# Kernel optimization log

Measured on AMD Instinct MI355X. Metric: run time of the kernel, lower is better.

The kernel has to match this reference:

```python
import jax, jax.numpy as jnp
import numpy as np

E = 8          # n_routed_experts
D = 2048       # model dim
I = 1408       # moe_inter_dim
K = 2          # n_activated_experts (top-k)
T = 4096       # num tokens


def setup_inputs() -> dict:
    key = jax.random.key(0)
    k1, k2, k3, k4, k5 = jax.random.split(key, 5)
    x = jax.random.normal(k1, (T, D), dtype=jnp.float32)
    token_mask = jnp.ones((T,), dtype=bool)
    weights = jax.random.uniform(k2, (T, K), dtype=jnp.float32)
    indices = jax.random.randint(k3, (T, K), 0, E)
    init_std = 0.02
    gate_and_up_projs = jax.random.normal(k4, (E, D, 2 * I), dtype=jnp.float32) * init_std
    down_projs = jax.random.normal(k5, (E, I, D), dtype=jnp.float32) * init_std
    return {
        "x": x,
        "token_mask": token_mask,
        "weights": weights,
        "indices": indices,
        "gate_and_up_projs": gate_and_up_projs,
        "down_projs": down_projs,
    }


def reference(x, token_mask, weights, indices, gate_and_up_projs, down_projs):
    # Per-expert gate+up projection over all tokens (dense equivalent of the
    # dispatch + grouped-GEMM): [E, T, 2I]
    gu = jnp.einsum("td,edh->eth", x, gate_and_up_projs)
    gate, up = jnp.split(gu, 2, axis=-1)          # swiglu uses torch.chunk(.., 2, -1)
    inter = jax.nn.silu(gate) * up                # [E, T, I]
    y = jnp.einsum("eti,eid->etd", inter, down_projs)  # [E, T, D]
    # Combine: masked tokens (indices filled to -1) contribute nothing -> zero weight
    w_eff = weights * token_mask[:, None].astype(weights.dtype)   # [T, K]
    tok = jnp.arange(T)
    gathered = y[indices, tok[:, None], :]        # [T, K, D]
    out = jnp.einsum("tk,tkd->td", w_eff, gathered)
    return out.astype(x.dtype)
```

## Files before the change

### kernel.cpp

```cpp
#include <hip/hip_runtime.h>
#include <hip/hip_bf16.h>
#include <cstdint>
#include <cstddef>

#define TT 4096
#define DD 2048
#define II 1408
#define EE 8
#define KK 2
#define H2 2816

#define MAXTILES 72
#define BK 32
#define LDK 40

typedef __bf16 bf16x8 __attribute__((ext_vector_type(8)));
typedef float  f32x4  __attribute__((ext_vector_type(4)));

static __device__ __forceinline__ unsigned short f2bf(float f) {
    union { float f; unsigned int u; } v; v.f = f;
    unsigned int u = v.u;
    u += 0x7fffu + ((u >> 16) & 1u);
    return (unsigned short)(u >> 16);
}

static __device__ __forceinline__ bf16x8 ld_frag(const unsigned short* p) {
    return *(const bf16x8*)p;
}

static __device__ __forceinline__ void gload16(const unsigned short* g, unsigned short* l) {
    __builtin_amdgcn_global_load_lds(
        (__attribute__((address_space(1))) void*)(g),
        (__attribute__((address_space(3))) void*)(l),
        16, 0, 0);
}

__global__ __launch_bounds__(256) void k_convert_x(const float* __restrict__ x,
                                                   unsigned short* __restrict__ xb) {
    size_t i = ((size_t)blockIdx.x * 256 + threadIdx.x) * 8;
    const float4* p = (const float4*)(x + i);
    float4 a = p[0], b = p[1];
    uint4 o;
    o.x = (unsigned)f2bf(a.x) | ((unsigned)f2bf(a.y) << 16);
    o.y = (unsigned)f2bf(a.z) | ((unsigned)f2bf(a.w) << 16);
    o.z = (unsigned)f2bf(b.x) | ((unsigned)f2bf(b.y) << 16);
    o.w = (unsigned)f2bf(b.z) | ((unsigned)f2bf(b.w) << 16);
    *(uint4*)(xb + i) = o;
}

__global__ __launch_bounds__(256) void k_tr_cvt(const float* __restrict__ src,
                                                unsigned short* __restrict__ dst,
                                                int K, int H) {
    __shared__ float tile[64][65];
    int e = blockIdx.z;
    int h0 = blockIdx.x * 64, k0 = blockIdx.y * 64;
    const float* s = src + (size_t)e * K * H;
    unsigned short* d = dst + (size_t)e * K * H;
    int t = threadIdx.x;
    #pragma unroll
    for (int i = 0; i < 4; i++) {
        int idx = t + i * 256;
        int r = idx >> 4, c = (idx & 15) * 4;
        float4 v = *(const float4*)(s + (size_t)(k0 + r) * H + h0 + c);
        tile[r][c] = v.x; tile[r][c + 1] = v.y; tile[r][c + 2] = v.z; tile[r][c + 3] = v.w;
    }
    __syncthreads();
    #pragma unroll
    for (int i = 0; i < 4; i++) {
        int idx = t + i * 256;
        int h = idx >> 4, c = (idx & 15) * 4;
        ushort4 o;
        o.x = f2bf(tile[c][h]);     o.y = f2bf(tile[c + 1][h]);
        o.z = f2bf(tile[c + 2][h]); o.w = f2bf(tile[c + 3][h]);
        *(ushort4*)(d + (size_t)(h0 + h) * K + k0 + c) = o;
    }
}

__global__ __launch_bounds__(256) void k_build_lists(const int* __restrict__ indices,
                                                     const float* __restrict__ weights,
                                                     int* __restrict__ cnt,
                                                     int* __restrict__ tok_slab,
                                                     float* __restrict__ w_slab) {
    int g = blockIdx.x * 256 + threadIdx.x;
    if (g >= TT * KK) return;
    int t = g >> 1;
    int e = indices[g];
    float w = weights[g];
    int pos = atomicAdd(&cnt[e], 1);
    tok_slab[e * (TT * KK) + pos] = t;
    w_slab[e * (TT * KK) + pos] = w;
}

__global__ __launch_bounds__(256) void k_build_tiles(const int* __restrict__ cnt,
                                                     const int* __restrict__ tok_slab,
                                                     const float* __restrict__ w_slab,
                                                     int* __restrict__ ctok,
                                                     float* __restrict__ cw,
                                                     int* __restrict__ tr0,
                                                     int* __restrict__ trows,
                                                     int* __restrict__ te) {
    __shared__ int s_off[EE];
    __shared__ int s_cnt[EE];
    if (threadIdx.x == 0) {
        int off = 0, nt = 0;
        for (int e = 0; e < EE; e++) {
            int c = cnt[e];
            s_off[e] = off; s_cnt[e] = c;
            int n = (c + 127) >> 7;
            for (int j = 0; j < n; j++) {
                tr0[nt]   = off + j * 128;
                trows[nt] = min(128, c - j * 128);
                te[nt]    = e;
                nt++;
            }
            off += c;
        }
        for (; nt < MAXTILES; nt++) trows[nt] = 0;
    }
    __syncthreads();
    for (int e = 0; e < EE; e++) {
        int c = s_cnt[e], base = s_off[e];
        for (int i = threadIdx.x; i < c; i += 256) {
            ctok[base + i] = tok_slab[e * (TT * KK) + i];
            cw[base + i]   = w_slab[e * (TT * KK) + i];
        }
    }
}


__global__ __launch_bounds__(256, 2) void k_gemm1_f(const unsigned short* __restrict__ xb,
                                                    const unsigned short* __restrict__ wt1,
                                                    const int* __restrict__ tr0,
                                                    const int* __restrict__ trows,
                                                    const int* __restrict__ te,
                                                    const int* __restrict__ ctok,
                                                    unsigned short* __restrict__ inter) {
    int tile = blockIdx.x;
    int rows = trows[tile];
    if (rows == 0) return;
    int row0 = tr0[tile], e = te[tile], n0 = blockIdx.y * 128;
    int tid = threadIdx.x, wave = tid >> 6, lane = tid & 63;

    __shared__ unsigned short As[128 * 32];
    __shared__ unsigned short Bg[128 * 32];
    __shared__ unsigned short Bu[128 * 32];
    __shared__ int toks[128];

    for (int i = tid; i < 128; i += 256) toks[i] = ctok[row0 + ((i < rows) ? i : 0)];
    __syncthreads();

    int rl = wave * 32 + (lane >> 2);
    int kc = (lane & 3) * 8;
    const unsigned short* gA0 = xb + (size_t)toks[rl] * DD + kc;
    const unsigned short* gA1 = xb + (size_t)toks[rl + 16] * DD + kc;
    const unsigned short* wte = wt1 + (size_t)e * H2 * DD;
    const unsigned short* gBg0 = wte + (size_t)(n0 + rl) * DD + kc;
    const unsigned short* gBg1 = wte + (size_t)(n0 + rl + 16) * DD + kc;
    const unsigned short* gBu0 = gBg0 + (size_t)II * DD;
    const unsigned short* gBu1 = gBg1 + (size_t)II * DD;

    unsigned short* lA0  = &As[(wave * 32) * 32];
    unsigned short* lA1  = &As[(wave * 32 + 16) * 32];
    unsigned short* lBg0 = &Bg[(wave * 32) * 32];
    unsigned short* lBg1 = &Bg[(wave * 32 + 16) * 32];
    unsigned short* lBu0 = &Bu[(wave * 32) * 32];
    unsigned short* lBu1 = &Bu[(wave * 32 + 16) * 32];

    int mb = (wave & 1) * 64, nb = (wave >> 1) * 64;
    int lrow = lane & 15, quad = lane >> 4;

    f32x4 accg[4][4], accu[4][4];
    #pragma unroll
    for (int i = 0; i < 4; i++)
        #pragma unroll
        for (int j = 0; j < 4; j++) { accg[i][j] = (f32x4){0,0,0,0}; accu[i][j] = (f32x4){0,0,0,0}; }

    #pragma unroll 1
    for (int k0 = 0; k0 < DD; k0 += BK) {
        __syncthreads();
        gload16(gA0, lA0);   gload16(gA1, lA1);
        gload16(gBg0, lBg0); gload16(gBg1, lBg1);
        gload16(gBu0, lBu0); gload16(gBu1, lBu1);
        gA0 += BK; gA1 += BK; gBg0 += BK; gBg1 += BK; gBu0 += BK; gBu1 += BK;
        __syncthreads();

        bf16x8 af[4], bg[4], bu[4];
        #pragma unroll
        for (int i = 0; i < 4; i++)
            af[i] = ld_frag(&As[(mb + i * 16 + lrow) * 32 + quad * 8]);
        #pragma unroll
        for (int j = 0; j < 4; j++) {
            bg[j] = ld_frag(&Bg[(nb + j * 16 + lrow) * 32 + quad * 8]);
            bu[j] = ld_frag(&Bu[(nb + j * 16 + lrow) * 32 + quad * 8]);
        }
        #pragma unroll
        for (int i = 0; i < 4; i++)
            #pragma unroll
            for (int j = 0; j < 4; j++) {
                accg[i][j] = __builtin_amdgcn_mfma_f32_16x16x32_bf16(af[i], bg[j], accg[i][j], 0, 0, 0);
                accu[i][j] = __builtin_amdgcn_mfma_f32_16x16x32_bf16(af[i], bu[j], accu[i][j], 0, 0, 0);
            }
    }

    #pragma unroll
    for (int i = 0; i < 4; i++) {
        int rl0 = mb + i * 16 + quad * 4;
        #pragma unroll
        for (int r = 0; r < 4; r++) {
            int rr = rl0 + r;
            if (rr < rows) {
                size_t base = (size_t)(row0 + rr) * II + n0 + nb;
                #pragma unroll
                for (int j = 0; j < 4; j++) {
                    float g = accg[i][j][r], u = accu[i][j][r];
                    float s = g / (1.0f + __expf(-g));
                    inter[base + j * 16 + lrow] = f2bf(s * u);
                }
            }
        }
    }
}

__global__ __launch_bounds__(256, 2) void k_gemm2_f(const unsigned short* __restrict__ inter,
                                                    const unsigned short* __restrict__ wt2,
                                                    const int* __restrict__ tr0,
                                                    const int* __restrict__ trows,
                                                    const int* __restrict__ te,
                                                    const int* __restrict__ ctok,
                                                    const float* __restrict__ cw,
                                                    float* __restrict__ out) {
    int tile = blockIdx.x;
    int rows = trows[tile];
    if (rows == 0) return;
    int row0 = tr0[tile], e = te[tile], n0 = blockIdx.y * 128;
    int tid = threadIdx.x, wave = tid >> 6, lane = tid & 63;

    __shared__ unsigned short As[128 * 32];
    __shared__ unsigned short Bs[128 * 32];
    __shared__ int   toks[128];
    __shared__ float wts[128];

    for (int i = tid; i < 128; i += 256) {
        bool v = (i < rows);
        toks[i] = v ? ctok[row0 + i] : -1;
        wts[i]  = v ? cw[row0 + i] : 0.0f;
    }
    __syncthreads();

    int rl = wave * 32 + (lane >> 2);
    int kc = (lane & 3) * 8;
    int r0c = (rl < rows) ? rl : 0;
    int r1c = (rl + 16 < rows) ? rl + 16 : 0;
    const unsigned short* gA0 = inter + (size_t)(row0 + r0c) * II + kc;
    const unsigned short* gA1 = inter + (size_t)(row0 + r1c) * II + kc;
    const unsigned short* wte = wt2 + (size_t)e * DD * II;
    const unsigned short* gB0 = wte + (size_t)(n0 + rl) * II + kc;
    const unsigned short* gB1 = wte + (size_t)(n0 + rl + 16) * II + kc;

    unsigned short* lA0 = &As[(wave * 32) * 32];
    unsigned short* lA1 = &As[(wave * 32 + 16) * 32];
    unsigned short* lB0 = &Bs[(wave * 32) * 32];
    unsigned short* lB1 = &Bs[(wave * 32 + 16) * 32];

    int mb = (wave & 1) * 64, nb = (wave >> 1) * 64;
    int lrow = lane & 15, quad = lane >> 4;

    f32x4 acc[4][4];
    #pragma unroll
    for (int i = 0; i < 4; i++)
        #pragma unroll
        for (int j = 0; j < 4; j++) acc[i][j] = (f32x4){0,0,0,0};

    #pragma unroll 1
    for (int k0 = 0; k0 < II; k0 += BK) {
        __syncthreads();
        gload16(gA0, lA0); gload16(gA1, lA1);
        gload16(gB0, lB0); gload16(gB1, lB1);
        gA0 += BK; gA1 += BK; gB0 += BK; gB1 += BK;
        __syncthreads();

        bf16x8 af[4], bfg[4];
        #pragma unroll
        for (int i = 0; i < 4; i++)
            af[i] = ld_frag(&As[(mb + i * 16 + lrow) * 32 + quad * 8]);
        #pragma unroll
        for (int j = 0; j < 4; j++)
            bfg[j] = ld_frag(&Bs[(nb + j * 16 + lrow) * 32 + quad * 8]);
        #pragma unroll
        for (int i = 0; i < 4; i++)
            #pragma unroll
            for (int j = 0; j < 4; j++)
                acc[i][j] = __builtin_amdgcn_mfma_f32_16x16x32_bf16(af[i], bfg[j], acc[i][j], 0, 0, 0);
    }

    #pragma unroll
    for (int i = 0; i < 4; i++) {
        int rl0 = mb + i * 16 + quad * 4;
        #pragma unroll
        for (int r = 0; r < 4; r++) {
            int rr = rl0 + r;
            if (rr < rows) {
                int t = toks[rr];
                float w = wts[rr];
                float* op = out + (size_t)t * DD + n0 + nb;
                #pragma unroll
                for (int j = 0; j < 4; j++)
                    unsafeAtomicAdd(op + j * 16 + lrow, w * acc[i][j][r]);
            }
        }
    }
}


__global__ __launch_bounds__(256, 2) void k_gemm1_s(const unsigned short* __restrict__ xb,
                                                    const float* __restrict__ gup,
                                                    const int* __restrict__ tr0,
                                                    const int* __restrict__ trows,
                                                    const int* __restrict__ te,
                                                    const int* __restrict__ ctok,
                                                    unsigned short* __restrict__ inter) {
    int tile = blockIdx.x;
    int rows = trows[tile];
    if (rows == 0) return;
    int row0 = tr0[tile];
    int e    = te[tile];
    int n0   = blockIdx.y * 128;
    int tid  = threadIdx.x;

    __shared__ unsigned short As[128 * LDK];
    __shared__ unsigned short Bg[128 * LDK];
    __shared__ unsigned short Bu[128 * LDK];
    __shared__ int toks[128];

    for (int i = tid; i < 128; i += 256) toks[i] = (i < rows) ? ctok[row0 + i] : -1;

    const float* Wbase = gup + (size_t)e * DD * H2;

    int wave = tid >> 6, lane = tid & 63;
    int mb = (wave & 1) * 64, nb = (wave >> 1) * 64;
    int lrow = lane & 15, quad = lane >> 4;

    f32x4 accg[4][4], accu[4][4];
    #pragma unroll
    for (int i = 0; i < 4; i++)
        #pragma unroll
        for (int j = 0; j < 4; j++) { accg[i][j] = (f32x4){0,0,0,0}; accu[i][j] = (f32x4){0,0,0,0}; }

    #pragma unroll 1
    for (int k0 = 0; k0 < DD; k0 += BK) {
        __syncthreads();
        #pragma unroll
        for (int c = tid; c < 512; c += 256) {
            int r = c >> 2, kk = (c & 3) << 3;
            uint4 v = make_uint4(0, 0, 0, 0);
            int t = toks[r];
            if (t >= 0) v = *(const uint4*)(xb + (size_t)t * DD + k0 + kk);
            *(uint4*)&As[r * LDK + kk] = v;
        }
        #pragma unroll
        for (int c = tid; c < 512; c += 256) {
            int n = c & 127, kcc = (c >> 7) << 3;
            const float* p = Wbase + (size_t)(k0 + kcc) * H2 + (n0 + n);
            unsigned short hg[8], hu[8];
            #pragma unroll
            for (int j = 0; j < 8; j++) {
                hg[j] = f2bf(p[(size_t)j * H2]);
                hu[j] = f2bf(p[(size_t)j * H2 + II]);
            }
            uint4 vg, vu;
            vg.x = (unsigned)hg[0] | ((unsigned)hg[1] << 16);
            vg.y = (unsigned)hg[2] | ((unsigned)hg[3] << 16);
            vg.z = (unsigned)hg[4] | ((unsigned)hg[5] << 16);
            vg.w = (unsigned)hg[6] | ((unsigned)hg[7] << 16);
            vu.x = (unsigned)hu[0] | ((unsigned)hu[1] << 16);
            vu.y = (unsigned)hu[2] | ((unsigned)hu[3] << 16);
            vu.z = (unsigned)hu[4] | ((unsigned)hu[5] << 16);
            vu.w = (unsigned)hu[6] | ((unsigned)hu[7] << 16);
            *(uint4*)&Bg[n * LDK + kcc] = vg;
            *(uint4*)&Bu[n * LDK + kcc] = vu;
        }
        __syncthreads();

        bf16x8 af[4], bg[4], bu[4];
        #pragma unroll
        for (int i = 0; i < 4; i++)
            af[i] = ld_frag(&As[(mb + i * 16 + lrow) * LDK + quad * 8]);
        #pragma unroll
        for (int j = 0; j < 4; j++) {
            bg[j] = ld_frag(&Bg[(nb + j * 16 + lrow) * LDK + quad * 8]);
            bu[j] = ld_frag(&Bu[(nb + j * 16 + lrow) * LDK + quad * 8]);
        }
        #pragma unroll
        for (int i = 0; i < 4; i++)
            #pragma unroll
            for (int j = 0; j < 4; j++) {
                accg[i][j] = __builtin_amdgcn_mfma_f32_16x16x32_bf16(af[i], bg[j], accg[i][j], 0, 0, 0);
                accu[i][j] = __builtin_amdgcn_mfma_f32_16x16x32_bf16(af[i], bu[j], accu[i][j], 0, 0, 0);
            }
    }

    #pragma unroll
    for (int i = 0; i < 4; i++) {
        int rl0 = mb + i * 16 + quad * 4;
        #pragma unroll
        for (int r = 0; r < 4; r++) {
            int rl = rl0 + r;
            if (rl < rows) {
                size_t base = (size_t)(row0 + rl) * II + n0 + nb;
                #pragma unroll
                for (int j = 0; j < 4; j++) {
                    float g = accg[i][j][r], u = accu[i][j][r];
                    float s = g / (1.0f + __expf(-g));
                    inter[base + j * 16 + lrow] = f2bf(s * u);
                }
            }
        }
    }
}

__global__ __launch_bounds__(256, 2) void k_gemm2_s(const unsigned short* __restrict__ inter,
                                                    const float* __restrict__ down,
                                                    const int* __restrict__ tr0,
                                                    const int* __restrict__ trows,
                                                    const int* __restrict__ te,
                                                    const int* __restrict__ ctok,
                                                    const float* __restrict__ cw,
                                                    float* __restrict__ out) {
    int tile = blockIdx.x;
    int rows = trows[tile];
    if (rows == 0) return;
    int row0 = tr0[tile];
    int e    = te[tile];
    int n0   = blockIdx.y * 128;
    int tid  = threadIdx.x;

    __shared__ unsigned short As[128 * LDK];
    __shared__ unsigned short Bs[128 * LDK];
    __shared__ int   toks[128];
    __shared__ float wts[128];

    for (int i = tid; i < 128; i += 256) {
        bool v = (i < rows);
        toks[i] = v ? ctok[row0 + i] : -1;
        wts[i]  = v ? cw[row0 + i] : 0.0f;
    }

    const float* Wbase = down + (size_t)e * II * DD;

    int wave = tid >> 6, lane = tid & 63;
    int mb = (wave & 1) * 64, nb = (wave >> 1) * 64;
    int lrow = lane & 15, quad = lane >> 4;

    f32x4 acc[4][4];
    #pragma unroll
    for (int i = 0; i < 4; i++)
        #pragma unroll
        for (int j = 0; j < 4; j++) acc[i][j] = (f32x4){0,0,0,0};

    #pragma unroll 1
    for (int k0 = 0; k0 < II; k0 += BK) {
        __syncthreads();
        #pragma unroll
        for (int c = tid; c < 512; c += 256) {
            int r = c >> 2, kk = (c & 3) << 3;
            uint4 v = make_uint4(0, 0, 0, 0);
            if (r < rows) v = *(const uint4*)(inter + (size_t)(row0 + r) * II + k0 + kk);
            *(uint4*)&As[r * LDK + kk] = v;
        }
        #pragma unroll
        for (int c = tid; c < 512; c += 256) {
            int n = c & 127, kcc = (c >> 7) << 3;
            const float* p = Wbase + (size_t)(k0 + kcc) * DD + (n0 + n);
            unsigned short h[8];
            #pragma unroll
            for (int j = 0; j < 8; j++) h[j] = f2bf(p[(size_t)j * DD]);
            uint4 v;
            v.x = (unsigned)h[0] | ((unsigned)h[1] << 16);
            v.y = (unsigned)h[2] | ((unsigned)h[3] << 16);
            v.z = (unsigned)h[4] | ((unsigned)h[5] << 16);
            v.w = (unsigned)h[6] | ((unsigned)h[7] << 16);
            *(uint4*)&Bs[n * LDK + kcc] = v;
        }
        __syncthreads();

        bf16x8 af[4], bfg[4];
        #pragma unroll
        for (int i = 0; i < 4; i++)
            af[i] = ld_frag(&As[(mb + i * 16 + lrow) * LDK + quad * 8]);
        #pragma unroll
        for (int j = 0; j < 4; j++)
            bfg[j] = ld_frag(&Bs[(nb + j * 16 + lrow) * LDK + quad * 8]);
        #pragma unroll
        for (int i = 0; i < 4; i++)
            #pragma unroll
            for (int j = 0; j < 4; j++)
                acc[i][j] = __builtin_amdgcn_mfma_f32_16x16x32_bf16(af[i], bfg[j], acc[i][j], 0, 0, 0);
    }

    #pragma unroll
    for (int i = 0; i < 4; i++) {
        int rl0 = mb + i * 16 + quad * 4;
        #pragma unroll
        for (int r = 0; r < 4; r++) {
            int rl = rl0 + r;
            if (rl < rows) {
                int t = toks[rl];
                float w = wts[rl];
                float* op = out + (size_t)t * DD + n0 + nb;
                #pragma unroll
                for (int j = 0; j < 4; j++)
                    unsafeAtomicAdd(op + j * 16 + lrow, w * acc[i][j][r]);
            }
        }
    }
}

constexpr size_t OFF_CNT   = 0;
constexpr size_t OFF_STOK  = 256;
constexpr size_t OFF_SW    = OFF_STOK + (size_t)EE * TT * KK * 4;
constexpr size_t OFF_CTOK  = OFF_SW + (size_t)EE * TT * KK * 4;
constexpr size_t OFF_CW    = OFF_CTOK + (size_t)TT * KK * 4;
constexpr size_t OFF_TR0   = OFF_CW + (size_t)TT * KK * 4;
constexpr size_t OFF_TRS   = OFF_TR0 + 512;
constexpr size_t OFF_TE    = OFF_TRS + 512;
constexpr size_t OFF_XB    = (OFF_TE + 512 + 255) & ~(size_t)255;
constexpr size_t OFF_INTER = OFF_XB + (size_t)TT * DD * 2;
constexpr size_t OFF_WT1   = OFF_INTER + (size_t)TT * KK * II * 2;
constexpr size_t OFF_WT2   = OFF_WT1 + (size_t)EE * H2 * DD * 2;
constexpr size_t WS_SLOW   = OFF_WT1;
constexpr size_t WS_FAST   = OFF_WT2 + (size_t)EE * DD * II * 2;

extern "C" void kernel_launch(void* const* d_in, const int* in_sizes, int n_in,
                              void* d_out, int out_size, void* d_ws, size_t ws_size,
                              hipStream_t stream) {
    const float* x       = (const float*)d_in[0];
    const float* weights = (const float*)d_in[2];
    const int*   indices = (const int*)d_in[3];
    const float* gup     = (const float*)d_in[4];
    const float* down    = (const float*)d_in[5];
    float* out = (float*)d_out;

    if (ws_size < WS_SLOW) return;

    char* ws = (char*)d_ws;
    int*            cnt      = (int*)(ws + OFF_CNT);
    int*            tok_slab = (int*)(ws + OFF_STOK);
    float*          w_slab   = (float*)(ws + OFF_SW);
    int*            ctok     = (int*)(ws + OFF_CTOK);
    float*          cw       = (float*)(ws + OFF_CW);
    int*            tr0      = (int*)(ws + OFF_TR0);
    int*            trows    = (int*)(ws + OFF_TRS);
    int*            te       = (int*)(ws + OFF_TE);
    unsigned short* xb       = (unsigned short*)(ws + OFF_XB);
    unsigned short* inter    = (unsigned short*)(ws + OFF_INTER);
    unsigned short* wt1      = (unsigned short*)(ws + OFF_WT1);
    unsigned short* wt2      = (unsigned short*)(ws + OFF_WT2);

    hipMemsetAsync(cnt, 0, EE * sizeof(int), stream);
    hipMemsetAsync(d_out, 0, (size_t)TT * DD * sizeof(float), stream);

    k_convert_x  <<<dim3((TT * DD) / (256 * 8)), 256, 0, stream>>>(x, xb);
    k_build_lists<<<dim3((TT * KK) / 256), 256, 0, stream>>>(indices, weights, cnt, tok_slab, w_slab);
    k_build_tiles<<<dim3(1), 256, 0, stream>>>(cnt, tok_slab, w_slab, ctok, cw, tr0, trows, te);

    if (ws_size >= WS_FAST) {
        k_tr_cvt<<<dim3(H2 / 64, DD / 64, EE), 256, 0, stream>>>(gup,  wt1, DD, H2);
        k_tr_cvt<<<dim3(DD / 64, II / 64, EE), 256, 0, stream>>>(down, wt2, II, DD);
        k_gemm1_f<<<dim3(MAXTILES, II / 128), 256, 0, stream>>>(xb, wt1, tr0, trows, te, ctok, inter);
        k_gemm2_f<<<dim3(MAXTILES, DD / 128), 256, 0, stream>>>(inter, wt2, tr0, trows, te, ctok, cw, out);
    } else {
        k_gemm1_s<<<dim3(MAXTILES, II / 128), 256, 0, stream>>>(xb, gup, tr0, trows, te, ctok, inter);
        k_gemm2_s<<<dim3(MAXTILES, DD / 128), 256, 0, stream>>>(inter, down, tr0, trows, te, ctok, cw, out);
    }
}
```

Before: 684.8 us.

## Replace atomic scatter-add in down GEMM with bf16 staging and combine kernel

The down-projection GEMM now writes per-pair results as bf16 into a compact buffer, placed in the weight workspace that is no longer needed. A new combine kernel gathers each token's two expert rows, applies the routing weights and writes the output directly. This removes the output memset and the float atomics on the output. In exchange it adds an extra 32MB write and read, and rounds expert outputs to bf16 before the weighted sum. The change also widens the transpose kernel's stores to 16 bytes and raises the GEMM launch bounds to three blocks per CU.

```diff
diff --git a/kernel.cpp b/kernel.cpp
--- a/kernel.cpp
+++ b/kernel.cpp
@@ -22,6 +22,10 @@
     unsigned int u = v.u;
     u += 0x7fffu + ((u >> 16) & 1u);
     return (unsigned short)(u >> 16);
+}
+
+static __device__ __forceinline__ float bfhi2f(unsigned int hi16) {
+    union { unsigned int u; float f; } v; v.u = hi16; return v.f;
 }
 
 static __device__ __forceinline__ bf16x8 ld_frag(const unsigned short* p) {
@@ -66,13 +70,19 @@
     }
     __syncthreads();
     #pragma unroll
-    for (int i = 0; i < 4; i++) {
+    for (int i = 0; i < 2; i++) {
         int idx = t + i * 256;
-        int h = idx >> 4, c = (idx & 15) * 4;
-        ushort4 o;
-        o.x = f2bf(tile[c][h]);     o.y = f2bf(tile[c + 1][h]);
-        o.z = f2bf(tile[c + 2][h]); o.w = f2bf(tile[c + 3][h]);
-        *(ushort4*)(d + (size_t)(h0 + h) * K + k0 + c) = o;
+        int h = idx >> 3;
+        int c = (idx & 7) * 8;
+        unsigned short o[8];
+        #pragma unroll
+        for (int j = 0; j < 8; j++) o[j] = f2bf(tile[c + j][h]);
+        uint4 v;
+        v.x = (unsigned)o[0] | ((unsigned)o[1] << 16);
+        v.y = (unsigned)o[2] | ((unsigned)o[3] << 16);
+        v.z = (unsigned)o[4] | ((unsigned)o[5] << 16);
+        v.w = (unsigned)o[6] | ((unsigned)o[7] << 16);
+        *(uint4*)(d + (size_t)(h0 + h) * K + k0 + c) = v;
     }
 }
 
@@ -80,7 +90,8 @@
                                                      const float* __restrict__ weights,
                                                      int* __restrict__ cnt,
                                                      int* __restrict__ tok_slab,
-                                                     float* __restrict__ w_slab) {
+                                                     float* __restrict__ w_slab,
+                                                     int* __restrict__ plocal) {
     int g = blockIdx.x * 256 + threadIdx.x;
     if (g >= TT * KK) return;
     int t = g >> 1;
@@ -89,6 +100,7 @@
     int pos = atomicAdd(&cnt[e], 1);
     tok_slab[e * (TT * KK) + pos] = t;
     w_slab[e * (TT * KK) + pos] = w;
+    plocal[g] = pos;
 }
 
 __global__ __launch_bounds__(256) void k_build_tiles(const int* __restrict__ cnt,
@@ -98,7 +110,8 @@
                                                      float* __restrict__ cw,
                                                      int* __restrict__ tr0,
                                                      int* __restrict__ trows,
-                                                     int* __restrict__ te) {
+                                                     int* __restrict__ te,
+                                                     int* __restrict__ eoff) {
     __shared__ int s_off[EE];
     __shared__ int s_cnt[EE];
     if (threadIdx.x == 0) {
@@ -106,6 +119,7 @@
         for (int e = 0; e < EE; e++) {
             int c = cnt[e];
             s_off[e] = off; s_cnt[e] = c;
+            eoff[e] = off;
             int n = (c + 127) >> 7;
             for (int j = 0; j < n; j++) {
                 tr0[nt]   = off + j * 128;
@@ -128,7 +142,7 @@
 }
 
 
-__global__ __launch_bounds__(256, 2) void k_gemm1_f(const unsigned short* __restrict__ xb,
+__global__ __launch_bounds__(256, 3) void k_gemm1_f(const unsigned short* __restrict__ xb,
                                                     const unsigned short* __restrict__ wt1,
                                                     const int* __restrict__ tr0,
                                                     const int* __restrict__ trows,
@@ -221,14 +235,12 @@
     }
 }
 
-__global__ __launch_bounds__(256, 2) void k_gemm2_f(const unsigned short* __restrict__ inter,
+__global__ __launch_bounds__(256, 3) void k_gemm2_f(const unsigned short* __restrict__ inter,
                                                     const unsigned short* __restrict__ wt2,
                                                     const int* __restrict__ tr0,
                                                     const int* __restrict__ trows,
                                                     const int* __restrict__ te,
-                                                    const int* __restrict__ ctok,
-                                                    const float* __restrict__ cw,
-                                                    float* __restrict__ out) {
+                                                    unsigned short* __restrict__ ypair) {
     int tile = blockIdx.x;
     int rows = trows[tile];
     if (rows == 0) return;
@@ -237,15 +249,6 @@
 
     __shared__ unsigned short As[128 * 32];
     __shared__ unsigned short Bs[128 * 32];
-    __shared__ int   toks[128];
-    __shared__ float wts[128];
-
-    for (int i = tid; i < 128; i += 256) {
-        bool v = (i < rows);
-        toks[i] = v ? ctok[row0 + i] : -1;
-        wts[i]  = v ? cw[row0 + i] : 0.0f;
-    }
-    __syncthreads();
 
     int rl = wave * 32 + (lane >> 2);
     int kc = (lane & 3) * 8;
@@ -300,15 +303,41 @@
         for (int r = 0; r < 4; r++) {
             int rr = rl0 + r;
             if (rr < rows) {
-                int t = toks[rr];
-                float w = wts[rr];
-                float* op = out + (size_t)t * DD + n0 + nb;
+                size_t base = (size_t)(row0 + rr) * DD + n0 + nb;
                 #pragma unroll
                 for (int j = 0; j < 4; j++)
-                    unsafeAtomicAdd(op + j * 16 + lrow, w * acc[i][j][r]);
-            }
-        }
-    }
+                    ypair[base + j * 16 + lrow] = f2bf(acc[i][j][r]);
+            }
+        }
+    }
+}
+
+__global__ __launch_bounds__(256) void k_combine(const unsigned short* __restrict__ ypair,
+                                                 const float* __restrict__ weights,
+                                                 const int* __restrict__ indices,
+                                                 const int* __restrict__ plocal,
+                                                 const int* __restrict__ eoff,
+                                                 float* __restrict__ out) {
+    int t = blockIdx.x;
+    int c = threadIdx.x * 8;
+    int g0 = 2 * t, g1 = 2 * t + 1;
+    int ci0 = eoff[indices[g0]] + plocal[g0];
+    int ci1 = eoff[indices[g1]] + plocal[g1];
+    float w0 = weights[g0], w1 = weights[g1];
+    uint4 a = *(const uint4*)(ypair + (size_t)ci0 * DD + c);
+    uint4 b = *(const uint4*)(ypair + (size_t)ci1 * DD + c);
+    float4 o0, o1;
+    o0.x = w0 * bfhi2f(a.x << 16) + w1 * bfhi2f(b.x << 16);
+    o0.y = w0 * bfhi2f(a.x & 0xffff0000u) + w1 * bfhi2f(b.x & 0xffff0000u);
+    o0.z = w0 * bfhi2f(a.y << 16) + w1 * bfhi2f(b.y << 16);
+    o0.w = w0 * bfhi2f(a.y & 0xffff0000u) + w1 * bfhi2f(b.y & 0xffff0000u);
+    o1.x = w0 * bfhi2f(a.z << 16) + w1 * bfhi2f(b.z << 16);
+    o1.y = w0 * bfhi2f(a.z & 0xffff0000u) + w1 * bfhi2f(b.z & 0xffff0000u);
+    o1.z = w0 * bfhi2f(a.w << 16) + w1 * bfhi2f(b.w << 16);
+    o1.w = w0 * bfhi2f(a.w & 0xffff0000u) + w1 * bfhi2f(b.w & 0xffff0000u);
+    float* op = out + (size_t)t * DD + c;
+    *(float4*)op = o0;
+    *(float4*)(op + 4) = o1;
 }
 
 
@@ -526,9 +555,12 @@
 constexpr size_t OFF_XB    = (OFF_TE + 512 + 255) & ~(size_t)255;
 constexpr size_t OFF_INTER = OFF_XB + (size_t)TT * DD * 2;
 constexpr size_t OFF_WT1   = OFF_INTER + (size_t)TT * KK * II * 2;
+constexpr size_t OFF_YP    = OFF_WT1;
 constexpr size_t OFF_WT2   = OFF_WT1 + (size_t)EE * H2 * DD * 2;
+constexpr size_t OFF_PLOC  = OFF_WT2 + (size_t)EE * DD * II * 2;
+constexpr size_t OFF_EOFF  = OFF_PLOC + (size_t)TT * KK * 4;
 constexpr size_t WS_SLOW   = OFF_WT1;
-constexpr size_t WS_FAST   = OFF_WT2 + (size_t)EE * DD * II * 2;
+constexpr size_t WS_FAST   = OFF_EOFF + 256;
 
 extern "C" void kernel_launch(void* const* d_in, const int* in_sizes, int n_in,
                               void* d_out, int out_size, void* d_ws, size_t ws_size,
@@ -554,21 +586,27 @@
     unsigned short* xb       = (unsigned short*)(ws + OFF_XB);
     unsigned short* inter    = (unsigned short*)(ws + OFF_INTER);
     unsigned short* wt1      = (unsigned short*)(ws + OFF_WT1);
+    unsigned short* ypair    = (unsigned short*)(ws + OFF_YP);
     unsigned short* wt2      = (unsigned short*)(ws + OFF_WT2);
+    int*            plocal   = (int*)(ws + OFF_PLOC);
+    int*            eoff     = (int*)(ws + OFF_EOFF);
 
     hipMemsetAsync(cnt, 0, EE * sizeof(int), stream);
-    hipMemsetAsync(d_out, 0, (size_t)TT * DD * sizeof(float), stream);
 
     k_convert_x  <<<dim3((TT * DD) / (256 * 8)), 256, 0, stream>>>(x, xb);
-    k_build_lists<<<dim3((TT * KK) / 256), 256, 0, stream>>>(indices, weights, cnt, tok_slab, w_slab);
-    k_build_tiles<<<dim3(1), 256, 0, stream>>>(cnt, tok_slab, w_slab, ctok, cw, tr0, trows, te);
 
     if (ws_size >= WS_FAST) {
+        k_build_lists<<<dim3((TT * KK) / 256), 256, 0, stream>>>(indices, weights, cnt, tok_slab, w_slab, plocal);
+        k_build_tiles<<<dim3(1), 256, 0, stream>>>(cnt, tok_slab, w_slab, ctok, cw, tr0, trows, te, eoff);
         k_tr_cvt<<<dim3(H2 / 64, DD / 64, EE), 256, 0, stream>>>(gup,  wt1, DD, H2);
         k_tr_cvt<<<dim3(DD / 64, II / 64, EE), 256, 0, stream>>>(down, wt2, II, DD);
         k_gemm1_f<<<dim3(MAXTILES, II / 128), 256, 0, stream>>>(xb, wt1, tr0, trows, te, ctok, inter);
-        k_gemm2_f<<<dim3(MAXTILES, DD / 128), 256, 0, stream>>>(inter, wt2, tr0, trows, te, ctok, cw, out);
+        k_gemm2_f<<<dim3(MAXTILES, DD / 128), 256, 0, stream>>>(inter, wt2, tr0, trows, te, ypair);
+        k_combine<<<dim3(TT), 256, 0, stream>>>(ypair, weights, indices, plocal, eoff, out);
     } else {
+        k_build_lists<<<dim3((TT * KK) / 256), 256, 0, stream>>>(indices, weights, cnt, tok_slab, w_slab, (int*)(ws + OFF_CTOK));
+        k_build_tiles<<<dim3(1), 256, 0, stream>>>(cnt, tok_slab, w_slab, ctok, cw, tr0, trows, te, (int*)(ws + OFF_CNT + 64));
+        hipMemsetAsync(d_out, 0, (size_t)TT * DD * sizeof(float), stream);
         k_gemm1_s<<<dim3(MAXTILES, II / 128), 256, 0, stream>>>(xb, gup, tr0, trows, te, ctok, inter);
         k_gemm2_s<<<dim3(MAXTILES, DD / 128), 256, 0, stream>>>(inter, down, tr0, trows, te, ctok, cw, out);
     }
```

Measured after the change: 837.7 us. +22.3%, slower.
